# Optimization experiments

Measured on AMD Instinct MI355X. Metric: run time of the kernel, lower is better.

## Reference

```python
import jax, jax.numpy as jnp
import numpy as np

NQ = 200000; K = 4; M = 64; KEY = 64; V = 128; E = 64; B = 512; S = 200

def setup_inputs() -> dict:
    key = jax.random.key(0)
    ks = jax.random.split(key, 16)
    return {
        'q_embed_table': jax.random.normal(ks[0], (NQ + 1, E), jnp.float32) * 0.1,
        'alpha_mean': jax.random.normal(ks[1], (NQ,), jnp.float32) * 0.2,
        'beta_base': jax.random.normal(ks[2], (NQ,), jnp.float32) * 0.5,
        'beta_gaps': jax.random.uniform(ks[3], (NQ, K - 2), jnp.float32) * 0.5 + 0.25,
        'ability_means': jax.random.normal(ks[4], (M, V), jnp.float32) * 0.1,
        'ability_log_vars': jnp.zeros((M, V), jnp.float32),
        'memory_keys': jax.random.normal(ks[5], (M, KEY), jnp.float32),
        'q_to_key_w': jax.random.normal(ks[6], (E, KEY), jnp.float32) / np.sqrt(E),
        'q_to_key_b': jnp.zeros((KEY,), jnp.float32),
        'qa_embed_w': jax.random.normal(ks[7], (2, E), jnp.float32),
        'qa_embed_b': jnp.zeros((E,), jnp.float32),
        'qa_to_ev_w': jax.random.normal(ks[8], (E, V), jnp.float32) / np.sqrt(E),
        'qa_to_ev_b': jnp.zeros((V,), jnp.float32),
        'questions': jax.random.randint(ks[9], (B, S), 0, NQ),
        'responses': jax.random.randint(ks[10], (B, S), 0, K),
    }


def reference(q_embed_table, alpha_mean, beta_base, beta_gaps, ability_means,
              ability_log_vars, memory_keys, q_to_key_w, q_to_key_b,
              qa_embed_w, qa_embed_b, qa_to_ev_w, qa_to_ev_b,
              questions, responses):
    nQ = alpha_mean.shape[0]
    Kc = beta_gaps.shape[1] + 2  # n_categories

    # --- gather question-specific IRT params (irregular gather) ---
    alphas = jnp.exp(alpha_mean[questions])                      # [B,S]
    base = beta_base[questions]                                  # [B,S]
    gaps = jax.nn.softplus(beta_gaps[questions])                 # [B,S,K-2]
    # cumulative thresholds: beta_0 = base, beta_k = beta_{k-1} + gap_{k-1}
    betas = jnp.cumsum(jnp.concatenate([base[..., None], gaps], axis=-1), axis=-1)  # [B,S,K-1]

    # --- attention over memory slots ---
    q_emb = q_embed_table[questions]                             # [B,S,E]
    queries = q_emb @ q_to_key_w + q_to_key_b                    # [B,S,KEY]
    attn = jax.nn.softmax(jnp.einsum('bsk,mk->bsm', queries, memory_keys), axis=-1)  # [B,S,M]

    # --- evidence embedding from (question, response) ---
    qn = questions.astype(jnp.float32) / nQ
    rn = responses.astype(jnp.float32) / (Kc - 1)
    qa = jnp.stack([qn, rn], axis=-1) @ qa_embed_w + qa_embed_b  # [B,S,E]
    evidence = jnp.tanh(qa) @ qa_to_ev_w + qa_to_ev_b            # [B,S,V]

    # --- sequential memory read + per-slot Bayesian scatter update ---
    def step(carry, inp):
        means, log_vars = carry                                  # [M,V] each
        attn_t, ev_t = inp                                       # [B,M], [B,V]
        theta = jnp.mean(attn_t @ means, axis=-1)                # bayesian_read -> [B]
        # precision-weighted update of every slot (evidence_precision = 1)
        w = jnp.mean(attn_t, axis=0)                             # [M] update weights
        ev_mean = jnp.mean(ev_t, axis=0)                         # [V]
        prior_prec = jnp.exp(-log_vars)
        post_prec = prior_prec + w[:, None]
        post_mean = (prior_prec * means + ev_mean[None, :] * w[:, None]) / post_prec
        # torch updates under no_grad -> stop_gradient
        new_means = jax.lax.stop_gradient(post_mean)
        new_lv = jax.lax.stop_gradient(-jnp.log(post_prec))
        return (new_means, new_lv), theta

    (_, _), thetas = jax.lax.scan(
        step, (ability_means, ability_log_vars),
        (attn.transpose(1, 0, 2), evidence.transpose(1, 0, 2)))
    thetas = thetas.T                                            # [B,S]

    # --- GPCM category probabilities ---
    z = alphas[..., None] * (thetas[..., None] - betas)          # [B,S,K-1]
    cum = jnp.concatenate([jnp.zeros_like(z[..., :1]), jnp.cumsum(z, axis=-1)], axis=-1)  # [B,S,K]
    probs = jax.nn.softmax(cum, axis=-1)
    return probs
```

## Files before the change

### kernel.cpp

```cpp
#include <hip/hip_runtime.h>
#include <math.h>

#define M_SLOTS 64
#define E_DIM   64
#define KEY_DIM 64
#define V_DIM   128
#define K_CAT   4
#define S_LEN   200

typedef __attribute__((ext_vector_type(8)))  short short8;
typedef __attribute__((ext_vector_type(16))) float f32x16;

#define OFF_CT     0
#define OFF_BM     2048
#define OFF_WBAR   2112
#define OFF_BBAR   2176
#define OFF_RM0    2240
#define OFF_P0     2304
#define OFF_WSUM   2368
#define OFF_EMSUM  (OFF_WSUM + S_LEN*M_SLOTS)
#define ZERO_CNT   (S_LEN*M_SLOTS + S_LEN)

__device__ __forceinline__ unsigned pk2rne(float lo, float hi) {
    unsigned ul = __float_as_uint(lo); ul += 0x7fffu + ((ul >> 16) & 1u);
    unsigned uh = __float_as_uint(hi); uh += 0x7fffu + ((uh >> 16) & 1u);
    return __builtin_amdgcn_perm(uh, ul, 0x07060302u);
}
__device__ __forceinline__ unsigned short bf16rne(float f) {
    unsigned u = __float_as_uint(f);
    return (unsigned short)((u + 0x7fffu + ((u >> 16) & 1u)) >> 16);
}
__device__ __forceinline__ short8 as_s8(uint4 u) { return __builtin_bit_cast(short8, u); }

__device__ __forceinline__ void gpcm_store(float th, int q,
                                           const float* __restrict__ alpha_mean,
                                           const float* __restrict__ beta_base,
                                           const float* __restrict__ beta_gaps,
                                           float* __restrict__ out, size_t idx) {
    float a  = __expf(alpha_mean[q]);
    float b0 = beta_base[q];
    float2 g = *reinterpret_cast<const float2*>(&beta_gaps[q * (K_CAT - 2)]);
    float g0 = log1pf(__expf(g.x));
    float g1 = log1pf(__expf(g.y));
    float be1 = b0 + g0;
    float be2 = be1 + g1;
    float z0 = a * (th - b0);
    float z1 = a * (th - be1);
    float z2 = a * (th - be2);
    float c1 = z0, c2 = z0 + z1, c3 = z0 + z1 + z2;
    float cm = fmaxf(fmaxf(0.f, c1), fmaxf(c2, c3));
    float e0 = __expf(0.f - cm), e1 = __expf(c1 - cm), e2 = __expf(c2 - cm), e3 = __expf(c3 - cm);
    float si = __fdividef(1.0f, e0 + e1 + e2 + e3);
    float4 o4 = make_float4(e0 * si, e1 * si, e2 * si, e3 * si);
    *reinterpret_cast<float4*>(&out[idx * K_CAT]) = o4;
}

__device__ __forceinline__ void load_qf(const float* __restrict__ qrow, int h, float4 qf[8]) {
    #pragma unroll
    for (int s = 0; s < 4; ++s) {
        const float4* src = (const float4*)(qrow + s * 16 + h * 8);
        qf[2 * s]     = src[0];
        qf[2 * s + 1] = src[1];
    }
}

__device__ __forceinline__ void load_afrags(const unsigned short* __restrict__ ct,
                                            int h, int p, uint4 af[8]) {
    #pragma unroll
    for (int mt = 0; mt < 2; ++mt)
        #pragma unroll
        for (int s = 0; s < 4; ++s)
            af[mt * 4 + s] = *(const uint4*)(ct + (p + 32 * mt) * E_DIM + s * 16 + h * 8);
}

__device__ __forceinline__ void mfma_logits(
    const float4 qf[8], const uint4 af[8],
    const float* __restrict__ bm, int h, f32x16 acc[2])
{
    #pragma unroll
    for (int mt = 0; mt < 2; ++mt)
        #pragma unroll
        for (int g = 0; g < 4; ++g) {
            float4 v = *(const float4*)(bm + 8 * g + 4 * h + 32 * mt);
            acc[mt][4 * g + 0] = v.x; acc[mt][4 * g + 1] = v.y;
            acc[mt][4 * g + 2] = v.z; acc[mt][4 * g + 3] = v.w;
        }
    #pragma unroll
    for (int s = 0; s < 4; ++s) {
        uint4 bf;
        bf.x = pk2rne(qf[2 * s].x,     qf[2 * s].y);
        bf.y = pk2rne(qf[2 * s].z,     qf[2 * s].w);
        bf.z = pk2rne(qf[2 * s + 1].x, qf[2 * s + 1].y);
        bf.w = pk2rne(qf[2 * s + 1].z, qf[2 * s + 1].w);
        short8 bfr = as_s8(bf);
        acc[0] = __builtin_amdgcn_mfma_f32_32x32x16_bf16(as_s8(af[s]),     bfr, acc[0], 0, 0, 0);
        acc[1] = __builtin_amdgcn_mfma_f32_32x32x16_bf16(as_s8(af[4 + s]), bfr, acc[1], 0, 0, 0);
    }
}

__device__ __forceinline__ void softmax_fold(
    const f32x16 acc[2], int lane, int h, float* lsFoldRow)
{
    float av[32];
    float ssum = 0.f;
    #pragma unroll
    for (int j = 0; j < 16; ++j) { av[j]      = __expf(acc[0][j]); ssum += av[j]; }
    #pragma unroll
    for (int j = 0; j < 16; ++j) { av[16 + j] = __expf(acc[1][j]); ssum += av[16 + j]; }
    ssum += __shfl_xor(ssum, 32);
    const float inv = __fdividef(1.0f, ssum);
    #pragma unroll
    for (int j = 0; j < 32; ++j) av[j] *= inv;
    #pragma unroll
    for (int step = 0; step < 5; ++step) {
        const int sh = 1 << step;
        #pragma unroll
        for (int j = 0; j < (32 >> step) / 2; ++j) {
            float p0 = av[2 * j]     + __shfl_xor(av[2 * j], sh);
            float p1 = av[2 * j + 1] + __shfl_xor(av[2 * j + 1], sh);
            av[j] = (lane & sh) ? p1 : p0;
        }
    }
    const int jj = lane & 31;
    const int m = (jj & 3) + 8 * ((jj >> 2) & 3) + 4 * h + 32 * (jj >> 4);
    lsFoldRow[m] = av[0];
}

__global__ __launch_bounds__(256) void k_pre(
    const float* __restrict__ q2k_w, const float* __restrict__ q2k_b,
    const float* __restrict__ mkeys,
    const float* __restrict__ ev_w, const float* __restrict__ ev_b,
    const float* __restrict__ means, const float* __restrict__ logvars,
    float* __restrict__ ws)
{
    const int tid = threadIdx.x;
    if (blockIdx.x != 0) {
        int i = ((int)blockIdx.x - 1) * 1024 + tid * 4;
        if (i + 4 <= ZERO_CNT) {
            *reinterpret_cast<float4*>(ws + OFF_WSUM + i) = make_float4(0.f, 0.f, 0.f, 0.f);
        } else {
            for (int j = i; j < ZERO_CNT; ++j) ws[OFF_WSUM + j] = 0.f;
        }
        return;
    }
    const int wv = tid >> 6, lane = tid & 63;
    const int h = lane >> 5, p = lane & 31;

    {
        const int m0 = (wv & 1) * 32, e0 = (wv >> 1) * 32;
        f32x16 d;
        #pragma unroll
        for (int i = 0; i < 16; ++i) d[i] = 0.f;
        #pragma unroll
        for (int s = 0; s < 4; ++s) {
            const float* ar = mkeys + (m0 + p) * KEY_DIM + s * 16 + h * 8;
            const float* br = q2k_w + (e0 + p) * KEY_DIM + s * 16 + h * 8;
            float4 a0 = *(const float4*)ar, a1 = *(const float4*)(ar + 4);
            float4 b0 = *(const float4*)br, b1 = *(const float4*)(br + 4);
            uint4 au, bu;
            au.x = pk2rne(a0.x, a0.y); au.y = pk2rne(a0.z, a0.w);
            au.z = pk2rne(a1.x, a1.y); au.w = pk2rne(a1.z, a1.w);
            bu.x = pk2rne(b0.x, b0.y); bu.y = pk2rne(b0.z, b0.w);
            bu.z = pk2rne(b1.x, b1.y); bu.w = pk2rne(b1.z, b1.w);
            d = __builtin_amdgcn_mfma_f32_32x32x16_bf16(as_s8(au), as_s8(bu), d, 0, 0, 0);
        }
        unsigned short* ct = (unsigned short*)ws;
        #pragma unroll
        for (int j = 0; j < 16; ++j) {
            int row = (j & 3) + 8 * ((j >> 2) & 3) + 4 * h;
            ct[(m0 + row) * E_DIM + e0 + p] = bf16rne(d[j]);
        }
    }

    if (wv == 0) {
        float s = 0.f;
        const float4* er = (const float4*)(ev_w + (size_t)lane * V_DIM);
        #pragma unroll
        for (int i = 0; i < V_DIM / 4; ++i) {
            float4 v = er[i];
            s += (v.x + v.y) + (v.z + v.w);
        }
        ws[OFF_WBAR + lane] = s * (1.0f / V_DIM);
    } else if (wv == 1) {
        float s = 0.f;
        const float4* mk = (const float4*)(mkeys + lane * KEY_DIM);
        const float4* qb = (const float4*)q2k_b;
        #pragma unroll
        for (int i = 0; i < KEY_DIM / 4; ++i) {
            float4 a = mk[i], c = qb[i];
            s += a.x * c.x + a.y * c.y + a.z * c.z + a.w * c.w;
        }
        ws[OFF_BM + lane] = s;
        float bbv = ev_b[lane] + ev_b[64 + lane];
        #pragma unroll
        for (int o = 32; o; o >>= 1) bbv += __shfl_xor(bbv, o);
        if (!lane) ws[OFF_BBAR] = bbv * (1.0f / V_DIM);
    } else if (wv == 2) {
        float s = 0.f;
        const float4* mr = (const float4*)(means + (size_t)lane * V_DIM);
        #pragma unroll
        for (int i = 0; i < V_DIM / 4; ++i) {
            float4 v = mr[i];
            s += (v.x + v.y) + (v.z + v.w);
        }
        ws[OFF_RM0 + lane] = s * (1.0f / V_DIM);
        ws[OFF_P0 + lane]  = __expf(-logvars[(size_t)lane * V_DIM]);
    }
}

__global__ __launch_bounds__(256, 3) void k_attn(
    const float* __restrict__ qtab, const int* __restrict__ qs, const int* __restrict__ rs,
    const float* __restrict__ ws_ro,
    const float* __restrict__ qa_w, const float* __restrict__ qa_b,
    float* __restrict__ wsum, float* __restrict__ emsum,
    int B, float invNQ)
{
    __shared__ float4 lsEv[64];
    __shared__ float lsFold[2][4][M_SLOTS];
    const int tid = threadIdx.x, wv = tid >> 6, lane = tid & 63;
    const int h = lane >> 5, p = lane & 31;
    const int t0 = blockIdx.x * 2, t1 = t0 + 1;
    const int b = blockIdx.y * 128 + wv * 32 + p;

    const int q0 = qs[(size_t)b * S_LEN + t0];
    const int r0 = rs[(size_t)b * S_LEN + t0];
    const int q1 = qs[(size_t)b * S_LEN + t1];
    const int r1 = rs[(size_t)b * S_LEN + t1];
    float4 qf0[8], qf1[8];
    load_qf(qtab + (size_t)q0 * E_DIM, h, qf0);
    load_qf(qtab + (size_t)q1 * E_DIM, h, qf1);

    uint4 af[8];
    load_afrags((const unsigned short*)ws_ro, h, p, af);

    if (tid < 64) lsEv[tid] = make_float4(qa_w[tid], qa_w[E_DIM + tid], qa_b[tid],
                                          ws_ro[OFF_WBAR + tid]);
    const float bb = ws_ro[OFF_BBAR];

    {
        f32x16 acc[2];
        mfma_logits(qf0, af, ws_ro + OFF_BM, h, acc);
        softmax_fold(acc, lane, h, &lsFold[0][wv][0]);
    }
    {
        f32x16 acc[2];
        mfma_logits(qf1, af, ws_ro + OFF_BM, h, acc);
        softmax_fold(acc, lane, h, &lsFold[1][wv][0]);
    }

    __syncthreads();

    if (wv < 2) {
        float s4 = (lsFold[wv][0][lane] + lsFold[wv][1][lane])
                 + (lsFold[wv][2][lane] + lsFold[wv][3][lane]);
        atomicAdd(&wsum[(wv ? t1 : t0) * M_SLOTS + lane], s4);
    }

    float ev0 = 0.f, ev1 = 0.f;
    const float qn0 = (float)q0 * invNQ, rn0 = (float)r0 * (1.0f / (K_CAT - 1));
    const float qn1 = (float)q1 * invNQ, rn1 = (float)r1 * (1.0f / (K_CAT - 1));
    #pragma unroll 8
    for (int e = 0; e < 32; ++e) {
        float4 pv = lsEv[h * 32 + e];
        float qa0 = fmaf(qn0, pv.x, fmaf(rn0, pv.y, pv.z));
        float qa1 = fmaf(qn1, pv.x, fmaf(rn1, pv.y, pv.z));
        float ez0 = __expf(2.0f * qa0);
        float ez1 = __expf(2.0f * qa1);
        ev0 = fmaf(__fdividef(ez0 - 1.0f, ez0 + 1.0f), pv.w, ev0);
        ev1 = fmaf(__fdividef(ez1 - 1.0f, ez1 + 1.0f), pv.w, ev1);
    }
    ev0 += __shfl_xor(ev0, 32); ev0 += bb;
    ev1 += __shfl_xor(ev1, 32); ev1 += bb;
    #pragma unroll
    for (int o = 16; o; o >>= 1) { ev0 += __shfl_xor(ev0, o); ev1 += __shfl_xor(ev1, o); }
    if (!lane) {
        atomicAdd(&emsum[t0], ev0);
        atomicAdd(&emsum[t1], ev1);
    }
}

__global__ __launch_bounds__(256, 3) void k_out(
    const float* __restrict__ qtab, const int* __restrict__ qs,
    const float* __restrict__ ws_ro,
    const float* __restrict__ alpha_mean, const float* __restrict__ beta_base,
    const float* __restrict__ beta_gaps, float* __restrict__ out, int B, float invB)
{
    __shared__ float lsW[4][M_SLOTS], lsN[4][M_SLOTS];
    __shared__ float lsRmP0[M_SLOTS], lsRmP1[M_SLOTS];
    const int tid = threadIdx.x, wv = tid >> 6, lane = tid & 63;
    const int h = lane >> 5, p = lane & 31;
    const int t0 = blockIdx.x * 2, t1 = t0 + 1;
    const int b = blockIdx.y * 128 + wv * 32 + p;

    const int q0 = qs[(size_t)b * S_LEN + t0];
    const int q1 = qs[(size_t)b * S_LEN + t1];
    float4 qf0[8], qf1[8];
    load_qf(qtab + (size_t)q0 * E_DIM, h, qf0);
    load_qf(qtab + (size_t)q1 * E_DIM, h, qf1);

    uint4 af[8];
    load_afrags((const unsigned short*)ws_ro, h, p, af);

    {
        const float* wsum  = ws_ro + OFF_WSUM;
        const float* emsum = ws_ro + OFF_EMSUM;
        const int seg = (t0 + 3) >> 2;
        const int s0 = wv * seg, s1 = min(s0 + seg, t0);
        float pw0 = 0.f, pn0 = 0.f, pw1 = 0.f, pn1 = 0.f;
        float pw2 = 0.f, pn2 = 0.f, pw3 = 0.f, pn3 = 0.f;
        int s = s0;
        for (; s + 4 <= s1; s += 4) {
            float w0 = wsum[(s + 0) * M_SLOTS + lane];
            float w1 = wsum[(s + 1) * M_SLOTS + lane];
            float w2 = wsum[(s + 2) * M_SLOTS + lane];
            float w3 = wsum[(s + 3) * M_SLOTS + lane];
            float e0 = emsum[s + 0], e1 = emsum[s + 1];
            float e2 = emsum[s + 2], e3 = emsum[s + 3];
            pw0 += w0; pn0 = fmaf(e0, w0, pn0);
            pw1 += w1; pn1 = fmaf(e1, w1, pn1);
            pw2 += w2; pn2 = fmaf(e2, w2, pn2);
            pw3 += w3; pn3 = fmaf(e3, w3, pn3);
        }
        for (; s < s1; ++s) {
            float w = wsum[s * M_SLOTS + lane];
            pw0 += w; pn0 = fmaf(emsum[s], w, pn0);
        }
        lsW[wv][lane] = (pw0 + pw1) + (pw2 + pw3);
        lsN[wv][lane] = (pn0 + pn1) + (pn2 + pn3);
    }
    __syncthreads();
    if (tid < 64) {
        const int m = tid;
        float sw = lsW[0][m] + lsW[1][m] + lsW[2][m] + lsW[3][m];
        float sn = lsN[0][m] + lsN[1][m] + lsN[2][m] + lsN[3][m];
        const float p0v = ws_ro[OFF_P0 + m];
        float den0 = p0v + sw * invB;
        float num0 = fmaf(p0v, ws_ro[OFF_RM0 + m], sn * (invB * invB));
        float wstep = ws_ro[OFF_WSUM + t0 * M_SLOTS + m];
        float estep = ws_ro[OFF_EMSUM + t0];
        float den1 = den0 + wstep * invB;
        float num1 = fmaf(estep * wstep, invB * invB, num0);
        const int idx = ((m >> 2) & 1) * 32 + ((m >> 5) & 1) * 16 + (m & 3) + 4 * ((m >> 3) & 3);
        lsRmP0[idx] = num0 / den0;
        lsRmP1[idx] = num1 / den1;
    }
    __syncthreads();

    #pragma unroll
    for (int it = 0; it < 2; ++it) {
        f32x16 acc[2];
        mfma_logits(it ? qf1 : qf0, af, ws_ro + OFF_BM, h, acc);
        const float* rmh = (it ? lsRmP1 : lsRmP0) + h * 32;
        float ssum = 0.f, th = 0.f;
        #pragma unroll
        for (int j = 0; j < 16; ++j) {
            float e = __expf(acc[0][j]);
            ssum += e;
            th = fmaf(e, rmh[j], th);
        }
        #pragma unroll
        for (int j = 0; j < 16; ++j) {
            float e = __expf(acc[1][j]);
            ssum += e;
            th = fmaf(e, rmh[16 + j], th);
        }
        ssum += __shfl_xor(ssum, 32);
        th   += __shfl_xor(th, 32);
        th = __fdividef(th, ssum);
        if (!h) {
            const int t = it ? t1 : t0;
            const int q = it ? q1 : q0;
            gpcm_store(th, q, alpha_mean, beta_base, beta_gaps, out, (size_t)b * S_LEN + t);
        }
    }
}

extern "C" void kernel_launch(void* const* d_in, const int* in_sizes, int n_in,
                              void* d_out, int out_size, void* d_ws, size_t ws_size,
                              hipStream_t stream) {
    const float* qtab       = (const float*)d_in[0];
    const float* alpha_mean = (const float*)d_in[1];
    const float* beta_base  = (const float*)d_in[2];
    const float* beta_gaps  = (const float*)d_in[3];
    const float* ab_means   = (const float*)d_in[4];
    const float* ab_logvars = (const float*)d_in[5];
    const float* mkeys      = (const float*)d_in[6];
    const float* q2k_w      = (const float*)d_in[7];
    const float* q2k_b      = (const float*)d_in[8];
    const float* qa_w       = (const float*)d_in[9];
    const float* qa_b       = (const float*)d_in[10];
    const float* ev_w       = (const float*)d_in[11];
    const float* ev_b       = (const float*)d_in[12];
    const int*   qs         = (const int*)d_in[13];
    const int*   rs         = (const int*)d_in[14];
    float* out = (float*)d_out;
    float* ws  = (float*)d_ws;

    const int NQ = in_sizes[1];
    const int S  = S_LEN;
    const int B  = in_sizes[13] / S;

    float* wsum  = ws + OFF_WSUM;
    float* emsum = ws + OFF_EMSUM;

    k_pre<<<14, 256, 0, stream>>>(q2k_w, q2k_b, mkeys, ev_w, ev_b,
                                  ab_means, ab_logvars, ws);

    dim3 g(S / 2, B / 128);
    k_attn<<<g, 256, 0, stream>>>(qtab, qs, rs, ws, qa_w, qa_b,
                                  wsum, emsum, B, 1.0f / (float)NQ);

    k_out<<<g, 256, 0, stream>>>(qtab, qs, ws, alpha_mean, beta_base,
                                 beta_gaps, out, B, 1.0f / (float)B);
}
```

Measured before the change: 44.45 us.

## Process four timesteps per block with double-buffered gathers and vector index loads

Each block in the attention and output kernels now handles four timesteps instead of two, halving the grid along the sequence axis. The question and response indices are read as one int4 per lane, and the embedding rows for the third and fourth steps are gathered into reused register buffers while earlier steps compute. All four waves now issue the wsum atomics, and per-step prefix reads in k_out amortize the historical-sum reduction over more steps. The cost is lower occupancy (launch bound relaxed to 2 blocks per CU), fewer blocks for latency hiding, and higher register pressure.

```diff
diff --git a/kernel.cpp b/kernel.cpp
--- a/kernel.cpp
+++ b/kernel.cpp
@@ -126,6 +126,34 @@
     lsFoldRow[m] = av[0];
 }
 
+__device__ __forceinline__ void out_one(
+    const float4 qf[8], const uint4 af[8], const float* __restrict__ bm,
+    const float* rmP , int h, int q,
+    const float* __restrict__ alpha_mean, const float* __restrict__ beta_base,
+    const float* __restrict__ beta_gaps, float* __restrict__ out, size_t idx)
+{
+    f32x16 acc[2];
+    mfma_logits(qf, af, bm, h, acc);
+    const float* rmh = rmP + h * 32;
+    float ssum = 0.f, th = 0.f;
+    #pragma unroll
+    for (int j = 0; j < 16; ++j) {
+        float e = __expf(acc[0][j]);
+        ssum += e;
+        th = fmaf(e, rmh[j], th);
+    }
+    #pragma unroll
+    for (int j = 0; j < 16; ++j) {
+        float e = __expf(acc[1][j]);
+        ssum += e;
+        th = fmaf(e, rmh[16 + j], th);
+    }
+    ssum += __shfl_xor(ssum, 32);
+    th   += __shfl_xor(th, 32);
+    th = __fdividef(th, ssum);
+    if (!h) gpcm_store(th, q, alpha_mean, beta_base, beta_gaps, out, idx);
+}
+
 __global__ __launch_bounds__(256) void k_pre(
     const float* __restrict__ q2k_w, const float* __restrict__ q2k_b,
     const float* __restrict__ mkeys,
@@ -208,7 +236,7 @@
     }
 }
 
-__global__ __launch_bounds__(256, 3) void k_attn(
+__global__ __launch_bounds__(256, 2) void k_attn(
     const float* __restrict__ qtab, const int* __restrict__ qs, const int* __restrict__ rs,
     const float* __restrict__ ws_ro,
     const float* __restrict__ qa_w, const float* __restrict__ qa_b,
@@ -216,19 +244,17 @@
     int B, float invNQ)
 {
     __shared__ float4 lsEv[64];
-    __shared__ float lsFold[2][4][M_SLOTS];
+    __shared__ float lsFold[4][4][M_SLOTS];
     const int tid = threadIdx.x, wv = tid >> 6, lane = tid & 63;
     const int h = lane >> 5, p = lane & 31;
-    const int t0 = blockIdx.x * 2, t1 = t0 + 1;
+    const int t0 = blockIdx.x * 4;
     const int b = blockIdx.y * 128 + wv * 32 + p;
 
-    const int q0 = qs[(size_t)b * S_LEN + t0];
-    const int r0 = rs[(size_t)b * S_LEN + t0];
-    const int q1 = qs[(size_t)b * S_LEN + t1];
-    const int r1 = rs[(size_t)b * S_LEN + t1];
-    float4 qf0[8], qf1[8];
-    load_qf(qtab + (size_t)q0 * E_DIM, h, qf0);
-    load_qf(qtab + (size_t)q1 * E_DIM, h, qf1);
+    const int4 qv = *reinterpret_cast<const int4*>(&qs[(size_t)b * S_LEN + t0]);
+    const int4 rv = *reinterpret_cast<const int4*>(&rs[(size_t)b * S_LEN + t0]);
+    float4 qfA[8], qfB[8];
+    load_qf(qtab + (size_t)qv.x * E_DIM, h, qfA);
+    load_qf(qtab + (size_t)qv.y * E_DIM, h, qfB);
 
     uint4 af[8];
     load_afrags((const unsigned short*)ws_ro, h, p, af);
@@ -236,67 +262,92 @@
     if (tid < 64) lsEv[tid] = make_float4(qa_w[tid], qa_w[E_DIM + tid], qa_b[tid],
                                           ws_ro[OFF_WBAR + tid]);
     const float bb = ws_ro[OFF_BBAR];
+    const float* bm = ws_ro + OFF_BM;
 
     {
         f32x16 acc[2];
-        mfma_logits(qf0, af, ws_ro + OFF_BM, h, acc);
+        mfma_logits(qfA, af, bm, h, acc);
         softmax_fold(acc, lane, h, &lsFold[0][wv][0]);
     }
+    load_qf(qtab + (size_t)qv.z * E_DIM, h, qfA);
     {
         f32x16 acc[2];
-        mfma_logits(qf1, af, ws_ro + OFF_BM, h, acc);
+        mfma_logits(qfB, af, bm, h, acc);
         softmax_fold(acc, lane, h, &lsFold[1][wv][0]);
     }
-
+    load_qf(qtab + (size_t)qv.w * E_DIM, h, qfB);
+    {
+        f32x16 acc[2];
+        mfma_logits(qfA, af, bm, h, acc);
+        softmax_fold(acc, lane, h, &lsFold[2][wv][0]);
+    }
+    {
+        f32x16 acc[2];
+        mfma_logits(qfB, af, bm, h, acc);
+        softmax_fold(acc, lane, h, &lsFold[3][wv][0]);
+    }
     __syncthreads();
 
-    if (wv < 2) {
+    {
         float s4 = (lsFold[wv][0][lane] + lsFold[wv][1][lane])
                  + (lsFold[wv][2][lane] + lsFold[wv][3][lane]);
-        atomicAdd(&wsum[(wv ? t1 : t0) * M_SLOTS + lane], s4);
-    }
-
-    float ev0 = 0.f, ev1 = 0.f;
-    const float qn0 = (float)q0 * invNQ, rn0 = (float)r0 * (1.0f / (K_CAT - 1));
-    const float qn1 = (float)q1 * invNQ, rn1 = (float)r1 * (1.0f / (K_CAT - 1));
+        atomicAdd(&wsum[(t0 + wv) * M_SLOTS + lane], s4);
+    }
+
+    float ev0 = 0.f, ev1 = 0.f, ev2 = 0.f, ev3 = 0.f;
+    const float kinv = 1.0f / (K_CAT - 1);
+    const float qn0 = (float)qv.x * invNQ, rn0 = (float)rv.x * kinv;
+    const float qn1 = (float)qv.y * invNQ, rn1 = (float)rv.y * kinv;
+    const float qn2 = (float)qv.z * invNQ, rn2 = (float)rv.z * kinv;
+    const float qn3 = (float)qv.w * invNQ, rn3 = (float)rv.w * kinv;
     #pragma unroll 8
     for (int e = 0; e < 32; ++e) {
         float4 pv = lsEv[h * 32 + e];
         float qa0 = fmaf(qn0, pv.x, fmaf(rn0, pv.y, pv.z));
         float qa1 = fmaf(qn1, pv.x, fmaf(rn1, pv.y, pv.z));
-        float ez0 = __expf(2.0f * qa0);
-        float ez1 = __expf(2.0f * qa1);
+        float qa2 = fmaf(qn2, pv.x, fmaf(rn2, pv.y, pv.z));
+        float qa3 = fmaf(qn3, pv.x, fmaf(rn3, pv.y, pv.z));
+        float ez0 = __expf(2.0f * qa0), ez1 = __expf(2.0f * qa1);
+        float ez2 = __expf(2.0f * qa2), ez3 = __expf(2.0f * qa3);
         ev0 = fmaf(__fdividef(ez0 - 1.0f, ez0 + 1.0f), pv.w, ev0);
         ev1 = fmaf(__fdividef(ez1 - 1.0f, ez1 + 1.0f), pv.w, ev1);
+        ev2 = fmaf(__fdividef(ez2 - 1.0f, ez2 + 1.0f), pv.w, ev2);
+        ev3 = fmaf(__fdividef(ez3 - 1.0f, ez3 + 1.0f), pv.w, ev3);
     }
     ev0 += __shfl_xor(ev0, 32); ev0 += bb;
     ev1 += __shfl_xor(ev1, 32); ev1 += bb;
-    #pragma unroll
-    for (int o = 16; o; o >>= 1) { ev0 += __shfl_xor(ev0, o); ev1 += __shfl_xor(ev1, o); }
+    ev2 += __shfl_xor(ev2, 32); ev2 += bb;
+    ev3 += __shfl_xor(ev3, 32); ev3 += bb;
+    #pragma unroll
+    for (int o = 16; o; o >>= 1) {
+        ev0 += __shfl_xor(ev0, o); ev1 += __shfl_xor(ev1, o);
+        ev2 += __shfl_xor(ev2, o); ev3 += __shfl_xor(ev3, o);
+    }
     if (!lane) {
-        atomicAdd(&emsum[t0], ev0);
-        atomicAdd(&emsum[t1], ev1);
-    }
-}
-
-__global__ __launch_bounds__(256, 3) void k_out(
+        atomicAdd(&emsum[t0 + 0], ev0);
+        atomicAdd(&emsum[t0 + 1], ev1);
+        atomicAdd(&emsum[t0 + 2], ev2);
+        atomicAdd(&emsum[t0 + 3], ev3);
+    }
+}
+
+__global__ __launch_bounds__(256, 2) void k_out(
     const float* __restrict__ qtab, const int* __restrict__ qs,
     const float* __restrict__ ws_ro,
     const float* __restrict__ alpha_mean, const float* __restrict__ beta_base,
     const float* __restrict__ beta_gaps, float* __restrict__ out, int B, float invB)
 {
     __shared__ float lsW[4][M_SLOTS], lsN[4][M_SLOTS];
-    __shared__ float lsRmP0[M_SLOTS], lsRmP1[M_SLOTS];
+    __shared__ float lsRmP[4][M_SLOTS];
     const int tid = threadIdx.x, wv = tid >> 6, lane = tid & 63;
     const int h = lane >> 5, p = lane & 31;
-    const int t0 = blockIdx.x * 2, t1 = t0 + 1;
+    const int t0 = blockIdx.x * 4;
     const int b = blockIdx.y * 128 + wv * 32 + p;
 
-    const int q0 = qs[(size_t)b * S_LEN + t0];
-    const int q1 = qs[(size_t)b * S_LEN + t1];
-    float4 qf0[8], qf1[8];
-    load_qf(qtab + (size_t)q0 * E_DIM, h, qf0);
-    load_qf(qtab + (size_t)q1 * E_DIM, h, qf1);
+    const int4 qv = *reinterpret_cast<const int4*>(&qs[(size_t)b * S_LEN + t0]);
+    float4 qfA[8], qfB[8];
+    load_qf(qtab + (size_t)qv.x * E_DIM, h, qfA);
+    load_qf(qtab + (size_t)qv.y * E_DIM, h, qfB);
 
     uint4 af[8];
     load_afrags((const unsigned short*)ws_ro, h, p, af);
@@ -334,45 +385,30 @@
         float sw = lsW[0][m] + lsW[1][m] + lsW[2][m] + lsW[3][m];
         float sn = lsN[0][m] + lsN[1][m] + lsN[2][m] + lsN[3][m];
         const float p0v = ws_ro[OFF_P0 + m];
-        float den0 = p0v + sw * invB;
-        float num0 = fmaf(p0v, ws_ro[OFF_RM0 + m], sn * (invB * invB));
-        float wstep = ws_ro[OFF_WSUM + t0 * M_SLOTS + m];
-        float estep = ws_ro[OFF_EMSUM + t0];
-        float den1 = den0 + wstep * invB;
-        float num1 = fmaf(estep * wstep, invB * invB, num0);
+        const float i2 = invB * invB;
+        float den = p0v + sw * invB;
+        float num = fmaf(p0v, ws_ro[OFF_RM0 + m], sn * i2);
         const int idx = ((m >> 2) & 1) * 32 + ((m >> 5) & 1) * 16 + (m & 3) + 4 * ((m >> 3) & 3);
-        lsRmP0[idx] = num0 / den0;
-        lsRmP1[idx] = num1 / den1;
+        lsRmP[0][idx] = num / den;
+        #pragma unroll
+        for (int k = 0; k < 3; ++k) {
+            float wstep = ws_ro[OFF_WSUM + (t0 + k) * M_SLOTS + m];
+            float estep = ws_ro[OFF_EMSUM + t0 + k];
+            den += wstep * invB;
+            num = fmaf(estep * wstep, i2, num);
+            lsRmP[k + 1][idx] = num / den;
+        }
     }
     __syncthreads();
 
-    #pragma unroll
-    for (int it = 0; it < 2; ++it) {
-        f32x16 acc[2];
-        mfma_logits(it ? qf1 : qf0, af, ws_ro + OFF_BM, h, acc);
-        const float* rmh = (it ? lsRmP1 : lsRmP0) + h * 32;
-        float ssum = 0.f, th = 0.f;
-        #pragma unroll
-        for (int j = 0; j < 16; ++j) {
-            float e = __expf(acc[0][j]);
-            ssum += e;
-            th = fmaf(e, rmh[j], th);
-        }
-        #pragma unroll
-        for (int j = 0; j < 16; ++j) {
-            float e = __expf(acc[1][j]);
-            ssum += e;
-            th = fmaf(e, rmh[16 + j], th);
-        }
-        ssum += __shfl_xor(ssum, 32);
-        th   += __shfl_xor(th, 32);
-        th = __fdividef(th, ssum);
-        if (!h) {
-            const int t = it ? t1 : t0;
-            const int q = it ? q1 : q0;
-            gpcm_store(th, q, alpha_mean, beta_base, beta_gaps, out, (size_t)b * S_LEN + t);
-        }
-    }
+    const float* bm = ws_ro + OFF_BM;
+    const size_t obase = (size_t)b * S_LEN;
+    out_one(qfA, af, bm, lsRmP[0], h, qv.x, alpha_mean, beta_base, beta_gaps, out, obase + t0);
+    load_qf(qtab + (size_t)qv.z * E_DIM, h, qfA);
+    out_one(qfB, af, bm, lsRmP[1], h, qv.y, alpha_mean, beta_base, beta_gaps, out, obase + t0 + 1);
+    load_qf(qtab + (size_t)qv.w * E_DIM, h, qfB);
+    out_one(qfA, af, bm, lsRmP[2], h, qv.z, alpha_mean, beta_base, beta_gaps, out, obase + t0 + 2);
+    out_one(qfB, af, bm, lsRmP[3], h, qv.w, alpha_mean, beta_base, beta_gaps, out, obase + t0 + 3);
 }
 
 extern "C" void kernel_launch(void* const* d_in, const int* in_sizes, int n_in,
@@ -406,7 +442,7 @@
     k_pre<<<14, 256, 0, stream>>>(q2k_w, q2k_b, mkeys, ev_w, ev_b,
                                   ab_means, ab_logvars, ws);
 
-    dim3 g(S / 2, B / 128);
+    dim3 g(S / 4, B / 128);
     k_attn<<<g, 256, 0, stream>>>(qtab, qs, rs, ws, qa_w, qa_b,
                                   wsum, emsum, B, 1.0f / (float)NQ);
 
```

After: 50.22 us. 13.0% more time.
